# Performance work log

Hardware: AMD Instinct MI355X
Metric: run time of the kernel (lower is better)

The kernel has to match this reference:

```python
import jax, jax.numpy as jnp
import numpy as np

EMBED = 1024
HEADS = 16
HEAD_DIM = EMBED // HEADS


def setup_inputs() -> dict:
    key = jax.random.key(0)
    ks = jax.random.split(key, 9)
    s = 1.0 / np.sqrt(EMBED)
    return {
        "x": jax.random.normal(ks[0], (4, 1024, EMBED), dtype=jnp.float32),
        "wq": jax.random.normal(ks[1], (EMBED, EMBED), dtype=jnp.float32) * s,
        "bq": jax.random.normal(ks[2], (EMBED,), dtype=jnp.float32) * s,
        "wk": jax.random.normal(ks[3], (EMBED, EMBED), dtype=jnp.float32) * s,
        "bk": jax.random.normal(ks[4], (EMBED,), dtype=jnp.float32) * s,
        "wv": jax.random.normal(ks[5], (EMBED, EMBED), dtype=jnp.float32) * s,
        "bv": jax.random.normal(ks[6], (EMBED,), dtype=jnp.float32) * s,
        "wo": jax.random.normal(ks[7], (EMBED, EMBED), dtype=jnp.float32) * s,
        "bo": jax.random.normal(ks[8], (EMBED,), dtype=jnp.float32) * s,
    }


def _split_heads(t):
    # (b, s, e) -> (b, h, s, d)
    b, s, _ = t.shape
    return t.reshape(b, s, HEADS, HEAD_DIM).transpose(0, 2, 1, 3)


def reference(x, wq, bq, wk, bk, wv, bv, wo, bo):
    # nn.Linear: y = x @ W.T + b
    q = _split_heads(x @ wq.T + bq)
    k = _split_heads(x @ wk.T + bk)
    v = _split_heads(x @ wv.T + bv)
    scale = 1.0 / jnp.sqrt(jnp.asarray(HEAD_DIM, dtype=x.dtype))
    scores = jnp.einsum("bhqd,bhkd->bhqk", q, k) * scale
    attn = jax.nn.softmax(scores, axis=-1)  # (b, h, s, s)
    ctx = jnp.einsum("bhqk,bhkd->bhqd", attn, v)
    b, h, s, d = ctx.shape
    ctx = ctx.transpose(0, 2, 1, 3).reshape(b, s, h * d)
    out = ctx @ wo.T + bo
    return out, attn
```

## Files before the change

### kernel.cpp

```cpp
#include <hip/hip_runtime.h>
#include <math.h>

#define BATCH 4
#define SEQ   1024
#define EMB   1024
#define HEADS 16
#define HD    64
#define MTOT  (BATCH*SEQ)

typedef float    f32x4 __attribute__((ext_vector_type(4)));
typedef float    vf4   __attribute__((ext_vector_type(4)));
typedef _Float16 f16;
typedef _Float16 f16x4 __attribute__((ext_vector_type(4)));
typedef _Float16 f16x8 __attribute__((ext_vector_type(8)));

__global__ __launch_bounds__(256) void convert_all(
    const float* __restrict__ x,
    const float* __restrict__ wq, const float* __restrict__ wk,
    const float* __restrict__ wv, const float* __restrict__ wo,
    f16* __restrict__ xh, f16* __restrict__ wh)
{
    const int bid = blockIdx.x;
    const float* src;
    f16* dst;
    if (bid < 4096) {
        src = x + ((size_t)bid << 10);
        dst = xh + ((size_t)bid << 10);
    } else {
        int t  = bid - 4096;
        int mi = t >> 10, r = t & 1023;
        const float* in = (mi == 0) ? wq : (mi == 1) ? wk : (mi == 2) ? wv : wo;
        src = in + ((size_t)r << 10);
        dst = wh + ((size_t)mi << 20) + ((size_t)r << 10);
    }
    int o = threadIdx.x << 2;
    float4 v = *(const float4*)(src + o);
    f16x4 h;
    h.x = (f16)v.x; h.y = (f16)v.y; h.z = (f16)v.z; h.w = (f16)v.w;
    *(f16x4*)(dst + o) = h;
}

#define BM  128
#define BN  128
#define LDT 72

__device__ __forceinline__ void mfma_gemm_tile(
    const f16* __restrict__ A, const f16* __restrict__ B,
    int m0, int n0, f32x4 acc[4][4], f16* SMEM)
{
    f16* As = SMEM;
    f16* Bs = SMEM + BM * LDT;
    const int tid  = threadIdx.x;
    const int lane = tid & 63;
    const int w    = tid >> 6;
    const int wr   = w >> 1, wc = w & 1;
    const int fr   = lane & 15;
    const int kb   = lane >> 4;

#pragma unroll
    for (int i = 0; i < 4; ++i)
#pragma unroll
        for (int j = 0; j < 4; ++j) acc[i][j] = (f32x4){0.f, 0.f, 0.f, 0.f};

    f16x8 ra[4], rb[4];
#define LOAD_STEP(KT)                                                          \
    {                                                                          \
        int k0 = (KT) * 64;                                                    \
        _Pragma("unroll")                                                      \
        for (int i = 0; i < 4; ++i) {                                          \
            int c = tid + (i << 8);                                            \
            int row = c >> 3, cc = (c & 7) << 3;                               \
            ra[i] = *(const f16x8*)(A + ((size_t)(m0 + row) << 10) + k0 + cc); \
            rb[i] = *(const f16x8*)(B + ((size_t)(n0 + row) << 10) + k0 + cc); \
        }                                                                      \
    }

    LOAD_STEP(0);
    for (int kt = 0; kt < 16; ++kt) {
        __syncthreads();
#pragma unroll
        for (int i = 0; i < 4; ++i) {
            int c = tid + (i << 8);
            int row = c >> 3, cc = (c & 7) << 3;
            *(f16x8*)&As[row * LDT + cc] = ra[i];
            *(f16x8*)&Bs[row * LDT + cc] = rb[i];
        }
        if (kt + 1 < 16) LOAD_STEP(kt + 1);
        __syncthreads();
#pragma unroll
        for (int kc = 0; kc < 2; ++kc) {
            f16x8 aF[4], bF[4];
#pragma unroll
            for (int i = 0; i < 4; ++i)
                aF[i] = *(const f16x8*)&As[(wr * 64 + i * 16 + fr) * LDT + kc * 32 + kb * 8];
#pragma unroll
            for (int j = 0; j < 4; ++j)
                bF[j] = *(const f16x8*)&Bs[(wc * 64 + j * 16 + fr) * LDT + kc * 32 + kb * 8];
#pragma unroll
            for (int i = 0; i < 4; ++i)
#pragma unroll
                for (int j = 0; j < 4; ++j)
                    acc[i][j] = __builtin_amdgcn_mfma_f32_16x16x32_f16(
                        aF[i], bF[j], acc[i][j], 0, 0, 0);
        }
    }
#undef LOAD_STEP
}

__global__ __launch_bounds__(256, 2) void qkv_mfma(
    const f16* __restrict__ xh, const f16* __restrict__ wh,
    const float* __restrict__ bq, const float* __restrict__ bk,
    const float* __restrict__ bv,
    f16* __restrict__ qh, f16* __restrict__ kh, f16* __restrict__ vf)
{
    __shared__ __align__(16) f16 SMEM[2 * BM * LDT];
    const int z = blockIdx.z;
    const f16* Bm = wh + ((size_t)z << 20);
    const float* bias = (z == 0) ? bq : (z == 1) ? bk : bv;
    const int m0 = blockIdx.y * BM, n0 = blockIdx.x * BN;
    f32x4 acc[4][4];
    mfma_gemm_tile(xh, Bm, m0, n0, acc, SMEM);

    const int tid  = threadIdx.x;
    const int lane = tid & 63;
    const int w    = tid >> 6;
    const int wr   = w >> 1, wc = w & 1;
    const int fr   = lane & 15;
    const int rg   = lane >> 4;
    const int LDC  = 136;
    const int b = m0 >> 10, sbase = m0 & 1023;

    __syncthreads();
    if (z < 2) {
        f16* p = (z == 0) ? qh : kh;
#pragma unroll
        for (int i = 0; i < 4; ++i)
#pragma unroll
            for (int j = 0; j < 4; ++j) {
                int nn = wc * 64 + j * 16 + fr;
                float bv_ = bias[n0 + nn];
#pragma unroll
                for (int r = 0; r < 4; ++r) {
                    int mm = wr * 64 + i * 16 + rg * 4 + r;
                    SMEM[mm * LDC + nn] = (f16)(acc[i][j][r] + bv_);
                }
            }
        __syncthreads();
#pragma unroll
        for (int t = 0; t < 8; ++t) {
            int idx = tid + (t << 8);
            int row = idx >> 4, ch = idx & 15;
            int n8 = n0 + ch * 8;
            int h = n8 >> 6, d = n8 & 63;
            f16x8 v = *(const f16x8*)&SMEM[row * LDC + ch * 8];
            *(f16x8*)(p + ((size_t)((b * HEADS + h) * SEQ + sbase + row)) * HD + d) = v;
        }
    } else {
#pragma unroll
        for (int i = 0; i < 4; ++i)
#pragma unroll
            for (int j = 0; j < 4; ++j) {
                int nn = wc * 64 + j * 16 + fr;
                float bv_ = bias[n0 + nn];
#pragma unroll
                for (int r = 0; r < 4; ++r) {
                    int mm = wr * 64 + i * 16 + rg * 4 + r;
                    SMEM[nn * LDC + mm] = (f16)(acc[i][j][r] + bv_);
                }
            }
        __syncthreads();
#pragma unroll
        for (int t = 0; t < 8; ++t) {
            int idx = tid + (t << 8);
            int mch = idx & 15;
            int col = idx >> 4;
            int n8 = n0 + col;
            int h = n8 >> 6, d = n8 & 63;
            int s0 = sbase + mch * 8;
            f16x8 v = *(const f16x8*)&SMEM[col * LDC + mch * 8];
            size_t a = ((size_t)(b * HEADS + h) << 16) +
                       (size_t)(s0 >> 5) * 2048 + d * 32 + (s0 & 31);
            *(f16x8*)(vf + a) = v;
        }
    }
}

__global__ __launch_bounds__(256, 2) void oproj_mfma(
    const f16* __restrict__ ch, const f16* __restrict__ wh,
    const float* __restrict__ bo, float* __restrict__ out)
{
    __shared__ __align__(16) f16 SMEM[2 * BM * LDT];
    const f16* Bm = wh + ((size_t)3 << 20);
    const int m0 = blockIdx.y * BM, n0 = blockIdx.x * BN;
    f32x4 acc[4][4];
    mfma_gemm_tile(ch, Bm, m0, n0, acc, SMEM);

    const int tid  = threadIdx.x;
    const int lane = tid & 63;
    const int w    = tid >> 6;
    const int wr   = w >> 1, wc = w & 1;
    const int fr   = lane & 15;
    const int rg   = lane >> 4;
    float* Cf = (float*)SMEM;
    const int LDCf = 132;

#pragma unroll
    for (int half = 0; half < 2; ++half) {
        __syncthreads();
        if (wr == half) {
#pragma unroll
            for (int i = 0; i < 4; ++i)
#pragma unroll
                for (int j = 0; j < 4; ++j) {
                    int nn = wc * 64 + j * 16 + fr;
                    float bv_ = bo[n0 + nn];
#pragma unroll
                    for (int r = 0; r < 4; ++r)
                        Cf[(i * 16 + rg * 4 + r) * LDCf + nn] = acc[i][j][r] + bv_;
                }
        }
        __syncthreads();
#pragma unroll
        for (int t = 0; t < 8; ++t) {
            int idx = tid + (t << 8);
            int row = idx >> 5, c4 = (idx & 31) << 2;
            vf4 v = *(const vf4*)&Cf[row * LDCf + c4];
            __builtin_nontemporal_store(v,
                (vf4*)(out + (size_t)(m0 + half * 64 + row) * EMB + n0 + c4));
        }
    }
}

__global__ __launch_bounds__(512, 4) void attn_kernel(
    const f16* __restrict__ qh, const f16* __restrict__ kh,
    const f16* __restrict__ vf,
    float* __restrict__ attn, f16* __restrict__ ch)
{
    __shared__ f16 SM[8192];
    __shared__ float RMAX[8][16];
    __shared__ float RSUM[8][16];

    const int lid = blockIdx.y * gridDim.x + blockIdx.x;
    const int xs  = lid & 7;
    const int jj  = lid >> 3;
    const int bh  = xs * 8 + (jj >> 5);
    const int qt  = jj & 31;

    const int tid  = threadIdx.x;
    const int w    = tid >> 6;
    const int grp  = w >> 2;
    const int wg   = w & 3;
    const int lane = tid & 63;
    const int c    = lane & 15;
    const int g    = lane >> 4;

    const size_t bhS = (size_t)bh * SEQ;
    const f16* VFb = vf + ((size_t)bh << 16);

    f16x8 Q0, Q1;
    {
        size_t qb = (bhS + qt * 32 + grp * 16 + c) * HD + g * 8;
        Q0 = *(const f16x8*)(qh + qb);
        Q1 = *(const f16x8*)(qh + qb + 32);
        Q0 *= (f16)0.125f;
        Q1 *= (f16)0.125f;
    }

    f32x4 s4[16];
#pragma unroll
    for (int kt = 0; kt < 16; ++kt) s4[kt] = (f32x4){0.f, 0.f, 0.f, 0.f};

    const int srow = tid >> 3;
    const int sch  = tid & 7;
    f16x8 kc0, kc1, kn0, kn1;
    {
        size_t ga = (bhS + srow) * HD + sch * 8;
        kc0 = *(const f16x8*)(kh + ga);
        kc1 = *(const f16x8*)(kh + ga + (size_t)64 * HD);
    }
#pragma unroll
    for (int kt2 = 0; kt2 < 8; ++kt2) {
        __syncthreads();
        {
            int r1 = srow + 64;
            *(f16x8*)&SM[srow * 64 + (sch ^ (srow & 7)) * 8] = kc0;
            *(f16x8*)&SM[r1 * 64 + (sch ^ (r1 & 7)) * 8]     = kc1;
        }
        if (kt2 < 7) {
            size_t ga = (bhS + (kt2 + 1) * 128 + srow) * HD + sch * 8;
            kn0 = *(const f16x8*)(kh + ga);
            kn1 = *(const f16x8*)(kh + ga + (size_t)64 * HD);
        }
        __syncthreads();
#pragma unroll
        for (int half = 0; half < 2; ++half) {
            const int krow = half * 64 + wg * 16 + c;
            const int ks7  = krow & 7;
            f16x8 B0 = *(const f16x8*)&SM[krow * 64 + ((0 + g) ^ ks7) * 8];
            f16x8 B1 = *(const f16x8*)&SM[krow * 64 + ((4 + g) ^ ks7) * 8];
            s4[kt2 * 2 + half] = __builtin_amdgcn_mfma_f32_16x16x32_f16(
                Q0, B0, s4[kt2 * 2 + half], 0, 0, 0);
            s4[kt2 * 2 + half] = __builtin_amdgcn_mfma_f32_16x16x32_f16(
                Q1, B1, s4[kt2 * 2 + half], 0, 0, 0);
        }
        kc0 = kn0; kc1 = kn1;
    }

    float m_[4], l_[4];
#pragma unroll
    for (int r = 0; r < 4; ++r) {
        float mm = -1e30f;
#pragma unroll
        for (int kt = 0; kt < 16; ++kt) mm = fmaxf(mm, s4[kt][r]);
        m_[r] = mm;
    }
#pragma unroll
    for (int off = 1; off < 16; off <<= 1)
#pragma unroll
        for (int r = 0; r < 4; ++r) m_[r] = fmaxf(m_[r], __shfl_xor(m_[r], off));
    if (c == 0) {
#pragma unroll
        for (int r = 0; r < 4; ++r) RMAX[w][g * 4 + r] = m_[r];
    }
    __syncthreads();
#pragma unroll
    for (int r = 0; r < 4; ++r)
        m_[r] = fmaxf(fmaxf(RMAX[grp * 4 + 0][g * 4 + r], RMAX[grp * 4 + 1][g * 4 + r]),
                      fmaxf(RMAX[grp * 4 + 2][g * 4 + r], RMAX[grp * 4 + 3][g * 4 + r]));
#pragma unroll
    for (int r = 0; r < 4; ++r) {
        float ss = 0.f;
#pragma unroll
        for (int kt = 0; kt < 16; ++kt) {
            float p = __expf(s4[kt][r] - m_[r]);
            s4[kt][r] = p;
            ss += p;
        }
        l_[r] = ss;
    }
#pragma unroll
    for (int off = 1; off < 16; off <<= 1)
#pragma unroll
        for (int r = 0; r < 4; ++r) l_[r] += __shfl_xor(l_[r], off);
    if (c == 0) {
#pragma unroll
        for (int r = 0; r < 4; ++r) RSUM[w][g * 4 + r] = l_[r];
    }
    __syncthreads();
#pragma unroll
    for (int r = 0; r < 4; ++r)
        l_[r] = 1.f / (RSUM[grp * 4 + 0][g * 4 + r] + RSUM[grp * 4 + 1][g * 4 + r] +
                       RSUM[grp * 4 + 2][g * 4 + r] + RSUM[grp * 4 + 3][g * 4 + r]);

    f32x4 ctx = (f32x4){0.f, 0.f, 0.f, 0.f};
    float* ap = attn + (bhS + qt * 32) * SEQ;
    const int dmy = wg * 16 + c;

#pragma unroll
    for (int ct = 0; ct < 8; ++ct) {
        f16x8 Vh[4];
#pragma unroll
        for (int ks = 0; ks < 4; ++ks)
            Vh[ks] = *(const f16x8*)(VFb + (ct * 4 + ks) * 2048 + dmy * 32 + g * 8);
        __syncthreads();
#pragma unroll
        for (int kt2 = 0; kt2 < 2; ++kt2) {
            const int ktg = ct * 2 + kt2;
            const int chh = (kt2 * 64 + wg * 16 + c) >> 3;
#pragma unroll
            for (int r = 0; r < 4; ++r) {
                const int q = g * 4 + r;
                float val = s4[ktg][r] * l_[r];
                int schP = chh ^ q;
                SM[(grp * 16 + q) * 128 + schP * 8 + (c & 7)] = (f16)val;
            }
        }
        __syncthreads();
#pragma unroll
        for (int ks = 0; ks < 4; ++ks) {
            f16x8 Pa = *(const f16x8*)&SM[(grp * 16 + c) * 128 + (((ks * 4 + g) ^ c) & 15) * 8];
            ctx = __builtin_amdgcn_mfma_f32_16x16x32_f16(Pa, Vh[ks], ctx, 0, 0, 0);
        }
#pragma unroll
        for (int t = 0; t < 2; ++t) {
            int idx = tid + (t << 9);
            int row = idx >> 5;
            int c4  = idx & 31;
            int col = c4 << 2;
            int swz = (col >> 3) ^ (row & 15);
            f16x4 pv = *(const f16x4*)&SM[row * 128 + swz * 8 + (col & 7)];
            vf4 o = __builtin_convertvector(pv, vf4);
            __builtin_nontemporal_store(o,
                (vf4*)(ap + (size_t)row * SEQ + ct * 128 + col));
        }
    }

    {
        int b = bh >> 4, h = bh & 15;
#pragma unroll
        for (int r = 0; r < 4; ++r) {
            int qrow = qt * 32 + grp * 16 + g * 4 + r;
            size_t a = (((size_t)(b * SEQ + qrow)) << 10) + h * HD + wg * 16 + c;
            ch[a] = (f16)ctx[r];
        }
    }
}

extern "C" void kernel_launch(void* const* d_in, const int* in_sizes, int n_in,
                              void* d_out, int out_size, void* d_ws, size_t ws_size,
                              hipStream_t stream) {
    const float* x  = (const float*)d_in[0];
    const float* wq = (const float*)d_in[1];
    const float* bq = (const float*)d_in[2];
    const float* wk = (const float*)d_in[3];
    const float* bk = (const float*)d_in[4];
    const float* wv = (const float*)d_in[5];
    const float* bv = (const float*)d_in[6];
    const float* wo = (const float*)d_in[7];
    const float* bo = (const float*)d_in[8];

    float* out      = (float*)d_out;
    float* attn_out = out + (size_t)BATCH * SEQ * EMB;

    const size_t MK = (size_t)MTOT * 1024;
    f16* ws16 = (f16*)d_ws;
    f16* xh = ws16;
    f16* wh = xh + MK;
    f16* qh = wh + ((size_t)4 << 20);
    f16* kh = qh + MK;
    f16* vf = kh + MK;
    f16* ch = xh;

    convert_all<<<8192, 256, 0, stream>>>(x, wq, wk, wv, wo, xh, wh);

    qkv_mfma<<<dim3(EMB / BN, MTOT / BM, 3), 256, 0, stream>>>(
        xh, wh, bq, bk, bv, qh, kh, vf);

    attn_kernel<<<dim3(SEQ / 32, BATCH * HEADS), 512, 0, stream>>>(
        qh, kh, vf, attn_out, ch);

    oproj_mfma<<<dim3(EMB / BN, MTOT / BM), 256, 0, stream>>>(
        ch, wh, bo, out);
}
```

Before: 140.6 us.

## Double-buffer K tiles and P tiles in shared memory inside attention kernel

Measured after the change: 146.8 us. +4.4%, slower.

```diff
diff --git a/kernel.cpp b/kernel.cpp
--- a/kernel.cpp
+++ b/kernel.cpp
@@ -236,7 +236,7 @@
     const f16* __restrict__ vf,
     float* __restrict__ attn, f16* __restrict__ ch)
 {
-    __shared__ f16 SM[8192];
+    __shared__ f16 SM[16384];
     __shared__ float RMAX[8][16];
     __shared__ float RSUM[8][16];
 
@@ -272,38 +272,49 @@
 
     const int srow = tid >> 3;
     const int sch  = tid & 7;
-    f16x8 kc0, kc1, kn0, kn1;
+    f16x8 kb0, kb1;
     {
         size_t ga = (bhS + srow) * HD + sch * 8;
-        kc0 = *(const f16x8*)(kh + ga);
-        kc1 = *(const f16x8*)(kh + ga + (size_t)64 * HD);
-    }
+        f16x8 a0 = *(const f16x8*)(kh + ga);
+        f16x8 a1 = *(const f16x8*)(kh + ga + (size_t)64 * HD);
+        int r1 = srow + 64;
+        *(f16x8*)&SM[srow * 64 + (sch ^ (srow & 7)) * 8] = a0;
+        *(f16x8*)&SM[r1 * 64 + (sch ^ (r1 & 7)) * 8]     = a1;
+    }
+    {
+        size_t ga = (bhS + 128 + srow) * HD + sch * 8;
+        kb0 = *(const f16x8*)(kh + ga);
+        kb1 = *(const f16x8*)(kh + ga + (size_t)64 * HD);
+    }
+    __syncthreads();
 #pragma unroll
     for (int kt2 = 0; kt2 < 8; ++kt2) {
-        __syncthreads();
-        {
-            int r1 = srow + 64;
-            *(f16x8*)&SM[srow * 64 + (sch ^ (srow & 7)) * 8] = kc0;
-            *(f16x8*)&SM[r1 * 64 + (sch ^ (r1 & 7)) * 8]     = kc1;
-        }
-        if (kt2 < 7) {
-            size_t ga = (bhS + (kt2 + 1) * 128 + srow) * HD + sch * 8;
-            kn0 = *(const f16x8*)(kh + ga);
-            kn1 = *(const f16x8*)(kh + ga + (size_t)64 * HD);
-        }
-        __syncthreads();
+        const int base = (kt2 & 1) * 8192;
+        __builtin_amdgcn_s_setprio(1);
 #pragma unroll
         for (int half = 0; half < 2; ++half) {
             const int krow = half * 64 + wg * 16 + c;
             const int ks7  = krow & 7;
-            f16x8 B0 = *(const f16x8*)&SM[krow * 64 + ((0 + g) ^ ks7) * 8];
-            f16x8 B1 = *(const f16x8*)&SM[krow * 64 + ((4 + g) ^ ks7) * 8];
+            f16x8 B0 = *(const f16x8*)&SM[base + krow * 64 + ((0 + g) ^ ks7) * 8];
+            f16x8 B1 = *(const f16x8*)&SM[base + krow * 64 + ((4 + g) ^ ks7) * 8];
             s4[kt2 * 2 + half] = __builtin_amdgcn_mfma_f32_16x16x32_f16(
                 Q0, B0, s4[kt2 * 2 + half], 0, 0, 0);
             s4[kt2 * 2 + half] = __builtin_amdgcn_mfma_f32_16x16x32_f16(
                 Q1, B1, s4[kt2 * 2 + half], 0, 0, 0);
         }
-        kc0 = kn0; kc1 = kn1;
+        __builtin_amdgcn_s_setprio(0);
+        if (kt2 < 7) {
+            const int nb = 8192 - base;
+            int r1 = srow + 64;
+            *(f16x8*)&SM[nb + srow * 64 + (sch ^ (srow & 7)) * 8] = kb0;
+            *(f16x8*)&SM[nb + r1 * 64 + (sch ^ (r1 & 7)) * 8]     = kb1;
+            if (kt2 < 6) {
+                size_t ga = (bhS + (kt2 + 2) * 128 + srow) * HD + sch * 8;
+                kb0 = *(const f16x8*)(kh + ga);
+                kb1 = *(const f16x8*)(kh + ga + (size_t)64 * HD);
+            }
+            __syncthreads();
+        }
     }
 
     float m_[4], l_[4];
@@ -356,44 +367,66 @@
     float* ap = attn + (bhS + qt * 32) * SEQ;
     const int dmy = wg * 16 + c;
 
+#define WRITE_PT(CTG, BASE)                                                    \
+    {                                                                          \
+        _Pragma("unroll")                                                      \
+        for (int kt2 = 0; kt2 < 2; ++kt2) {                                    \
+            const int ktg = (CTG) * 2 + kt2;                                   \
+            const int chh = (kt2 * 64 + wg * 16 + c) >> 3;                     \
+            _Pragma("unroll")                                                  \
+            for (int r = 0; r < 4; ++r) {                                      \
+                const int q = g * 4 + r;                                       \
+                float val = s4[ktg][r] * l_[r];                                \
+                int schP = chh ^ q;                                            \
+                SM[(BASE) + (grp * 16 + q) * 128 + schP * 8 + (c & 7)] =       \
+                    (f16)val;                                                  \
+            }                                                                  \
+        }                                                                      \
+    }
+
+    f16x8 Va[4], Vb[4];
+#pragma unroll
+    for (int ks = 0; ks < 4; ++ks)
+        Va[ks] = *(const f16x8*)(VFb + ks * 2048 + dmy * 32 + g * 8);
+    WRITE_PT(0, 0);
+    __syncthreads();
+
 #pragma unroll
     for (int ct = 0; ct < 8; ++ct) {
-        f16x8 Vh[4];
-#pragma unroll
-        for (int ks = 0; ks < 4; ++ks)
-            Vh[ks] = *(const f16x8*)(VFb + (ct * 4 + ks) * 2048 + dmy * 32 + g * 8);
-        __syncthreads();
-#pragma unroll
-        for (int kt2 = 0; kt2 < 2; ++kt2) {
-            const int ktg = ct * 2 + kt2;
-            const int chh = (kt2 * 64 + wg * 16 + c) >> 3;
-#pragma unroll
-            for (int r = 0; r < 4; ++r) {
-                const int q = g * 4 + r;
-                float val = s4[ktg][r] * l_[r];
-                int schP = chh ^ q;
-                SM[(grp * 16 + q) * 128 + schP * 8 + (c & 7)] = (f16)val;
-            }
-        }
-        __syncthreads();
+        const int pb = (ct & 1) * 4096;
+        if (ct < 7) {
+#pragma unroll
+            for (int ks = 0; ks < 4; ++ks)
+                Vb[ks] = *(const f16x8*)(VFb + ((ct + 1) * 4 + ks) * 2048 +
+                                         dmy * 32 + g * 8);
+        }
+        __builtin_amdgcn_s_setprio(1);
 #pragma unroll
         for (int ks = 0; ks < 4; ++ks) {
-            f16x8 Pa = *(const f16x8*)&SM[(grp * 16 + c) * 128 + (((ks * 4 + g) ^ c) & 15) * 8];
-            ctx = __builtin_amdgcn_mfma_f32_16x16x32_f16(Pa, Vh[ks], ctx, 0, 0, 0);
-        }
+            f16x8 Pa = *(const f16x8*)&SM[pb + (grp * 16 + c) * 128 +
+                                          (((ks * 4 + g) ^ c) & 15) * 8];
+            ctx = __builtin_amdgcn_mfma_f32_16x16x32_f16(Pa, Va[ks], ctx, 0, 0, 0);
+        }
+        __builtin_amdgcn_s_setprio(0);
 #pragma unroll
         for (int t = 0; t < 2; ++t) {
             int idx = tid + (t << 9);
             int row = idx >> 5;
-            int c4  = idx & 31;
-            int col = c4 << 2;
+            int col = (idx & 31) << 2;
             int swz = (col >> 3) ^ (row & 15);
-            f16x4 pv = *(const f16x4*)&SM[row * 128 + swz * 8 + (col & 7)];
+            f16x4 pv = *(const f16x4*)&SM[pb + row * 128 + swz * 8 + (col & 7)];
             vf4 o = __builtin_convertvector(pv, vf4);
             __builtin_nontemporal_store(o,
                 (vf4*)(ap + (size_t)row * SEQ + ct * 128 + col));
         }
-    }
+        if (ct < 7) {
+            WRITE_PT(ct + 1, 4096 - pb);
+            __syncthreads();
+        }
+#pragma unroll
+        for (int ks = 0; ks < 4; ++ks) Va[ks] = Vb[ks];
+    }
+#undef WRITE_PT
 
     {
         int b = bh >> 4, h = bh & 15;
```
